# Kernel optimization log

Measured on AMD Instinct MI355X. Metric: run time of the kernel, lower is better.

## Reference

```python
import jax, jax.numpy as jnp
import numpy as np

B, N, C, H = 8, 4096, 512, 8
HD = C // H  # head_dim = 64
SCALE = HD ** -0.5


def setup_inputs() -> dict:
    key = jax.random.key(0)
    k1, k2, k3, k4 = jax.random.split(key, 4)
    x1 = jax.random.normal(k1, (B, N, C), dtype=jnp.float32)
    x2 = jax.random.normal(k2, (B, N, C), dtype=jnp.float32)
    # nn.Linear(dim, 2*dim, bias=False) weights; stored as [in, out] for x @ W
    lim = 1.0 / np.sqrt(C)
    W_kv1 = jax.random.uniform(k3, (C, 2 * C), dtype=jnp.float32, minval=-lim, maxval=lim)
    W_kv2 = jax.random.uniform(k4, (C, 2 * C), dtype=jnp.float32, minval=-lim, maxval=lim)
    return {"x1": x1, "x2": x2, "W_kv1": W_kv1, "W_kv2": W_kv2}


def _heads(t):
    # [B, N, C] -> [B, H, N, HD]
    return t.reshape(B, N, H, HD).transpose(0, 2, 1, 3)


def _kv(x, W):
    kv = (x @ W).reshape(B, N, 2, H, HD)  # [B, N, 2, H, HD]
    kv = kv.transpose(2, 0, 3, 1, 4)      # [2, B, H, N, HD]
    return kv[0], kv[1]


def _ctx(k, v):
    # K^T V: [B, H, HD, HD], scaled then softmax over axis -2 (the k-feature axis)
    ctx = jnp.einsum("bhnd,bhne->bhde", k, v) * SCALE
    return jax.nn.softmax(ctx, axis=-2)


def reference(x1, x2, W_kv1, W_kv2):
    q1 = _heads(x1)
    q2 = _heads(x2)
    k1, v1 = _kv(x1, W_kv1)
    k2, v2 = _kv(x2, W_kv2)
    ctx1 = _ctx(k1, v1)
    ctx2 = _ctx(k2, v2)
    # cross: q1 attends via ctx2, q2 via ctx1
    o1 = jnp.einsum("bhnd,bhde->bhne", q1, ctx2).transpose(0, 2, 1, 3).reshape(B, N, C)
    o2 = jnp.einsum("bhnd,bhde->bhne", q2, ctx1).transpose(0, 2, 1, 3).reshape(B, N, C)
    return o1, o2
```

## Files before the change

### kernel.cpp

```cpp
#include <hip/hip_runtime.h>
#include <stdint.h>
#include <stddef.h>

#define NB 8
#define NSEQ 4096
#define NC 512
#define NH 8

typedef __attribute__((ext_vector_type(4))) float f4;
typedef __attribute__((ext_vector_type(8))) short bf8;
typedef __attribute__((ext_vector_type(4))) short bf4;

__device__ __forceinline__ short f2bf(float f) {
  union { float f; unsigned int u; } v; v.f = f;
  unsigned int u = v.u + 0x7FFFu + ((v.u >> 16) & 1u);
  return (short)(u >> 16);
}
__device__ __forceinline__ float bf2f(short h) {
  union { unsigned int u; float f; } v;
  v.u = ((unsigned int)(unsigned short)h) << 16;
  return v.f;
}

__global__ __launch_bounds__(256) void k_wt(const float* __restrict__ W0,
                                            const float* __restrict__ W1,
                                            short* __restrict__ Wth,
                                            short* __restrict__ Wtl) {
  __shared__ float t[64 * 65];
  int bid = blockIdx.x;
  int ot = bid & 15;
  int ct = (bid >> 4) & 7;
  int s = bid >> 7;
  const float* W = s ? W1 : W0;
  const float* src = W + (size_t)(ct * 64) * 1024 + ot * 64;
  int tid = threadIdx.x;
  int rr = tid >> 4, c4 = (tid & 15) * 4;
#pragma unroll
  for (int p = 0; p < 4; ++p) {
    int c = p * 16 + rr;
    f4 v = *(const f4*)&src[(size_t)c * 1024 + c4];
#pragma unroll
    for (int i = 0; i < 4; ++i) t[(c4 + i) * 65 + c] = v[i];
  }
  __syncthreads();
  size_t obase = (size_t)s * 524288 + (size_t)(ot * 64) * 512 + ct * 64;
#pragma unroll
  for (int p = 0; p < 4; ++p) {
    int o = p * 16 + rr;
    bf4 vh, vl;
#pragma unroll
    for (int i = 0; i < 4; ++i) {
      float v = t[o * 65 + c4 + i];
      short h = f2bf(v);
      vh[i] = h; vl[i] = f2bf(v - bf2f(h));
    }
    *(bf4*)&Wth[obase + (size_t)o * 512 + c4] = vh;
    *(bf4*)&Wtl[obase + (size_t)o * 512 + c4] = vl;
  }
}

__global__ __launch_bounds__(256) void k_xbt(const float* __restrict__ x0,
                                             const float* __restrict__ x1,
                                             short* __restrict__ XbT) {
  __shared__ short t[64 * 64];
  int bx = blockIdx.x;
  int ct = bx & 7;
  int nt = (bx >> 3) & 63;
  int b  = (bx >> 9) & 7;
  int s  = bx >> 12;
  const float* x = s ? x1 : x0;
  const float* xb = x + ((size_t)b * NSEQ + (size_t)nt * 64) * NC + ct * 64;
  int tid = threadIdx.x;
  int tn = tid >> 4;
  int tc = (tid & 15) * 4;
#pragma unroll
  for (int r = 0; r < 4; ++r) {
    int n = tn + r * 16;
    f4 v = *(const f4*)&xb[(size_t)n * NC + tc];
#pragma unroll
    for (int i = 0; i < 4; ++i) {
      int c = tc + i;
      int swz = (c & 7) ^ ((c >> 3) & 7);
      int byteoff = c * 128 + ((n * 2) ^ (swz << 4));
      t[byteoff >> 1] = f2bf(v[i]);
    }
  }
  __syncthreads();
  short* Xp = XbT + ((size_t)(s * 8 + b) * NC + (size_t)ct * 64) * NSEQ + (size_t)nt * 64;
  int ng4 = (tid & 15) * 4;
  int crb = tid >> 4;
#pragma unroll
  for (int r = 0; r < 4; ++r) {
    int cr = crb + r * 16;
    int swz = (cr & 7) ^ ((cr >> 3) & 7);
    int byteoff = cr * 128 + ((ng4 * 2) ^ (swz << 4));
    bf4 vv = *(const bf4*)&t[byteoff >> 1];
    *(bf4*)&Xp[(size_t)cr * NSEQ + ng4] = vv;
  }
}

__global__ __launch_bounds__(256) void k_gram(const short* __restrict__ XbT,
                                              float* __restrict__ G32) {
  __shared__ short Ab[2][64 * 64];
  __shared__ short Bb[2][64 * 64];
  int bid = blockIdx.x;
  int xcd = bid & 7;
  int j = bid >> 3;
  int sb = xcd + ((j >= 36) ? 8 : 0);
  int p = (j >= 36) ? (j - 36) : j;
  int ti = 0;
  while (p >= 8 - ti) { p -= 8 - ti; ++ti; }
  int tj = ti + p;
  int diag = (ti == tj);
  const short* Ar = XbT + ((size_t)sb * NC + ti * 64) * NSEQ;
  const short* Br = XbT + ((size_t)sb * NC + tj * 64) * NSEQ;
  int tid = threadIdx.x;
  int lane = tid & 63;
  int w = tid >> 6;
  int lrow = lane >> 3;
  int lgr = lane & 7;
  int wr = w & 1, wc = w >> 1;
  int mrow = lane & 15;
  int kreg = lane >> 4;
  f4 z = {0.f, 0.f, 0.f, 0.f};
  f4 acc[2][2];
#pragma unroll
  for (int i = 0; i < 2; ++i)
#pragma unroll
    for (int jj = 0; jj < 2; ++jj) acc[i][jj] = z;

  auto stage = [&](int buf, int k0) {
#pragma unroll
    for (int q = 0; q < 2; ++q) {
      int row = q * 32 + w * 8 + lrow;
      int gsw = (lgr ^ lrow) << 3;
      __builtin_amdgcn_global_load_lds((const unsigned int*)(Ar + (size_t)row * NSEQ + k0 + gsw),
                                       (unsigned int*)&Ab[buf][(q * 32 + w * 8) * 64], 16, 0, 0);
      if (!diag)
        __builtin_amdgcn_global_load_lds((const unsigned int*)(Br + (size_t)row * NSEQ + k0 + gsw),
                                         (unsigned int*)&Bb[buf][(q * 32 + w * 8) * 64], 16, 0, 0);
    }
  };
  auto comp = [&](int buf) {
    const short* Abuf = Ab[buf];
    const short* Bbuf = diag ? Ab[buf] : Bb[buf];
#pragma unroll
    for (int kk = 0; kk < 2; ++kk) {
      int gr = kk * 4 + kreg;
      bf8 a[2], b[2];
#pragma unroll
      for (int i = 0; i < 2; ++i) {
        int ra = wr * 32 + i * 16 + mrow;
        a[i] = *(const bf8*)&Abuf[ra * 64 + ((gr ^ (ra & 7)) << 3)];
        int rb2 = wc * 32 + i * 16 + mrow;
        b[i] = *(const bf8*)&Bbuf[rb2 * 64 + ((gr ^ (rb2 & 7)) << 3)];
      }
#pragma unroll
      for (int i = 0; i < 2; ++i)
#pragma unroll
        for (int jj = 0; jj < 2; ++jj)
          acc[i][jj] = __builtin_amdgcn_mfma_f32_16x16x32_bf16(a[i], b[jj], acc[i][jj], 0, 0, 0);
    }
  };

  stage(0, 0);
  __syncthreads();
  int cur = 0;
  for (int it = 0; it < 63; ++it) {
    stage(cur ^ 1, (it + 1) * 64);
    comp(cur);
    __syncthreads();
    cur ^= 1;
  }
  comp(cur);

  float* Gp = G32 + (size_t)sb * NC * NC;
  int rb = ti * 64 + wr * 32 + (lane >> 4) * 4;
  int cb = tj * 64 + wc * 32 + (lane & 15);
#pragma unroll
  for (int i = 0; i < 2; ++i)
#pragma unroll
    for (int jj = 0; jj < 2; ++jj)
#pragma unroll
      for (int r = 0; r < 4; ++r)
        Gp[(size_t)(rb + i * 16 + r) * NC + cb + jj * 16] = acc[i][jj][r];
}

__global__ __launch_bounds__(256) void k_sym(const float* __restrict__ G32,
                                             short* __restrict__ Gh,
                                             short* __restrict__ Gl) {
  __shared__ float t[64 * 65];
  int bid = blockIdx.x;
  int tile = bid & 63;
  int sb = bid >> 6;
  int ti = tile >> 3, tj = tile & 7;
  int tr = ti > tj;
  const float* src = G32 + (size_t)sb * 262144
                   + (tr ? ((size_t)(tj * 64) * 512 + ti * 64)
                         : ((size_t)(ti * 64) * 512 + tj * 64));
  int tid = threadIdx.x;
  int rr = tid >> 4;
  int c4 = (tid & 15) * 4;
#pragma unroll
  for (int p = 0; p < 4; ++p) {
    int r = p * 16 + rr;
    f4 v = *(const f4*)&src[(size_t)r * 512 + c4];
    if (tr) {
#pragma unroll
      for (int i = 0; i < 4; ++i) t[(c4 + i) * 65 + r] = v[i];
    } else {
#pragma unroll
      for (int i = 0; i < 4; ++i) t[r * 65 + c4 + i] = v[i];
    }
  }
  __syncthreads();
  size_t obase = (size_t)sb * 262144 + (size_t)(ti * 64) * 512 + tj * 64;
#pragma unroll
  for (int p = 0; p < 4; ++p) {
    int r = p * 16 + rr;
    bf4 vh, vl;
#pragma unroll
    for (int i = 0; i < 4; ++i) {
      float v = t[r * 65 + c4 + i] * 0.125f;
      short h = f2bf(v);
      vh[i] = h; vl[i] = f2bf(v - bf2f(h));
    }
    *(bf4*)&Gh[obase + (size_t)r * 512 + c4] = vh;
    *(bf4*)&Gl[obase + (size_t)r * 512 + c4] = vl;
  }
}

__global__ __launch_bounds__(256) void k_t(const short* __restrict__ Wth,
                                           const short* __restrict__ Wtl,
                                           const short* __restrict__ Gh,
                                           const short* __restrict__ Gl,
                                           float* __restrict__ Ttf) {
  __shared__ short Ah[128 * 40];
  __shared__ short Al[128 * 40];
  __shared__ short Bh[128 * 40];
  __shared__ short Bl[128 * 40];
  int tid = threadIdx.x;
  int et = blockIdx.x & 3;
  int ct = blockIdx.x >> 2;
  int sb = blockIdx.y;
  int s = sb >> 3;
  const short* Avh = Wth + ((size_t)s * 1024 + 512 + (size_t)et * 128) * NC;
  const short* Avl = Wtl + ((size_t)s * 1024 + 512 + (size_t)et * 128) * NC;
  const short* Gph = Gh + (size_t)sb * 262144 + (size_t)(ct * 128) * 512;
  const short* Gpl = Gl + (size_t)sb * 262144 + (size_t)(ct * 128) * 512;
  int cc = tid >> 1;
  int kh = (tid & 1) * 16;
  int lane = tid & 63;
  int w = tid >> 6;
  int wm = (w & 1) * 64;
  int wn = (w >> 1) * 64;
  int mrow = lane & 15;
  int kcol = (lane >> 4) * 8;
  f4 z = {0.f, 0.f, 0.f, 0.f};
  f4 acc[4][4];
#pragma unroll
  for (int i = 0; i < 4; ++i)
#pragma unroll
    for (int j = 0; j < 4; ++j) acc[i][j] = z;

  for (int it = 0; it < 16; ++it) {
    int k0 = it * 32;
    __syncthreads();
    *(bf8*)&Ah[cc * 40 + kh]     = *(const bf8*)&Avh[(size_t)cc * NC + k0 + kh];
    *(bf8*)&Ah[cc * 40 + kh + 8] = *(const bf8*)&Avh[(size_t)cc * NC + k0 + kh + 8];
    *(bf8*)&Al[cc * 40 + kh]     = *(const bf8*)&Avl[(size_t)cc * NC + k0 + kh];
    *(bf8*)&Al[cc * 40 + kh + 8] = *(const bf8*)&Avl[(size_t)cc * NC + k0 + kh + 8];
    *(bf8*)&Bh[cc * 40 + kh]     = *(const bf8*)&Gph[(size_t)cc * 512 + k0 + kh];
    *(bf8*)&Bh[cc * 40 + kh + 8] = *(const bf8*)&Gph[(size_t)cc * 512 + k0 + kh + 8];
    *(bf8*)&Bl[cc * 40 + kh]     = *(const bf8*)&Gpl[(size_t)cc * 512 + k0 + kh];
    *(bf8*)&Bl[cc * 40 + kh + 8] = *(const bf8*)&Gpl[(size_t)cc * 512 + k0 + kh + 8];
    __syncthreads();
    bf8 ah[4], al[4], bh[4], bl[4];
#pragma unroll
    for (int i = 0; i < 4; ++i) {
      ah[i] = *(const bf8*)&Ah[(wm + i * 16 + mrow) * 40 + kcol];
      al[i] = *(const bf8*)&Al[(wm + i * 16 + mrow) * 40 + kcol];
      bh[i] = *(const bf8*)&Bh[(wn + i * 16 + mrow) * 40 + kcol];
      bl[i] = *(const bf8*)&Bl[(wn + i * 16 + mrow) * 40 + kcol];
    }
#pragma unroll
    for (int i = 0; i < 4; ++i)
#pragma unroll
      for (int j = 0; j < 4; ++j) {
        acc[i][j] = __builtin_amdgcn_mfma_f32_16x16x32_bf16(ah[i], bh[j], acc[i][j], 0, 0, 0);
        acc[i][j] = __builtin_amdgcn_mfma_f32_16x16x32_bf16(ah[i], bl[j], acc[i][j], 0, 0, 0);
        acc[i][j] = __builtin_amdgcn_mfma_f32_16x16x32_bf16(al[i], bh[j], acc[i][j], 0, 0, 0);
      }
  }
  float* Tp = Ttf + (size_t)sb * NC * NC;
  int rb = et * 128 + wm + (lane >> 4) * 4;
  int cb = ct * 128 + wn + (lane & 15);
#pragma unroll
  for (int i = 0; i < 4; ++i)
#pragma unroll
    for (int j = 0; j < 4; ++j)
#pragma unroll
      for (int r = 0; r < 4; ++r)
        Tp[(size_t)(rb + i * 16 + r) * NC + cb + j * 16] = acc[i][j][r];
}

__global__ __launch_bounds__(256) void k_ctx(const short* __restrict__ Wth,
                                             const short* __restrict__ Wtl,
                                             const float* __restrict__ Ttf,
                                             short* __restrict__ ctxT) {
  __shared__ short Ah[64 * 72];
  __shared__ short Al[64 * 72];
  __shared__ short Bh[64 * 72];
  __shared__ short Bl[64 * 72];
  __shared__ float Sf[64 * 68];
  int tid = threadIdx.x;
  int h = blockIdx.x & 7;
  int sb = blockIdx.x >> 3;
  int s = sb >> 3;
  const short* Akh = Wth + ((size_t)s * 1024 + (size_t)h * 64) * NC;
  const short* Akl = Wtl + ((size_t)s * 1024 + (size_t)h * 64) * NC;
  const float* Bt = Ttf + ((size_t)sb * NC + (size_t)h * 64) * NC;
  int cs = tid >> 3;
  int kg = (tid & 7) * 8;
  int lane = tid & 63;
  int w = tid >> 6;
  int mrow = lane & 15;
  int kcol = (lane >> 4) * 8;
  f4 z = {0.f, 0.f, 0.f, 0.f};
  f4 acc[4];
#pragma unroll
  for (int j = 0; j < 4; ++j) acc[j] = z;

  for (int it = 0; it < 8; ++it) {
    int k0 = it * 64;
    __syncthreads();
#pragma unroll
    for (int r = 0; r < 2; ++r) {
      int d = cs + r * 32;
      *(bf8*)&Ah[d * 72 + kg] = *(const bf8*)&Akh[(size_t)d * NC + k0 + kg];
      *(bf8*)&Al[d * 72 + kg] = *(const bf8*)&Akl[(size_t)d * NC + k0 + kg];
      f4 g0 = *(const f4*)&Bt[(size_t)d * NC + k0 + kg];
      f4 g1 = *(const f4*)&Bt[(size_t)d * NC + k0 + kg + 4];
      bf8 vh, vl;
#pragma unroll
      for (int i = 0; i < 4; ++i) {
        short hh = f2bf(g0[i]);
        vh[i] = hh; vl[i] = f2bf(g0[i] - bf2f(hh));
        hh = f2bf(g1[i]);
        vh[i + 4] = hh; vl[i + 4] = f2bf(g1[i] - bf2f(hh));
      }
      *(bf8*)&Bh[d * 72 + kg] = vh;
      *(bf8*)&Bl[d * 72 + kg] = vl;
    }
    __syncthreads();
#pragma unroll
    for (int kk = 0; kk < 2; ++kk) {
      bf8 ah = *(const bf8*)&Ah[(w * 16 + mrow) * 72 + kk * 32 + kcol];
      bf8 al = *(const bf8*)&Al[(w * 16 + mrow) * 72 + kk * 32 + kcol];
#pragma unroll
      for (int j = 0; j < 4; ++j) {
        bf8 bh = *(const bf8*)&Bh[(j * 16 + mrow) * 72 + kk * 32 + kcol];
        bf8 bl = *(const bf8*)&Bl[(j * 16 + mrow) * 72 + kk * 32 + kcol];
        acc[j] = __builtin_amdgcn_mfma_f32_16x16x32_bf16(ah, bh, acc[j], 0, 0, 0);
        acc[j] = __builtin_amdgcn_mfma_f32_16x16x32_bf16(ah, bl, acc[j], 0, 0, 0);
        acc[j] = __builtin_amdgcn_mfma_f32_16x16x32_bf16(al, bh, acc[j], 0, 0, 0);
      }
    }
  }
  __syncthreads();
#pragma unroll
  for (int j = 0; j < 4; ++j)
#pragma unroll
    for (int r = 0; r < 4; ++r)
      Sf[(w * 16 + (lane >> 4) * 4 + r) * 68 + j * 16 + (lane & 15)] = acc[j][r];
  __syncthreads();
  if (tid < 64) {
    int e = tid;
    float mx = -1e30f;
    for (int d = 0; d < 64; ++d) mx = fmaxf(mx, Sf[d * 68 + e]);
    float sum = 0.f;
    for (int d = 0; d < 64; ++d) {
      float ev = __expf(Sf[d * 68 + e] - mx);
      sum += ev;
      Sf[d * 68 + e] = ev;
    }
    float rs = 1.f / sum;
    short* cp = ctxT + (((size_t)sb * NH + h) * 64 + e) * 64;
    for (int d0 = 0; d0 < 64; d0 += 4) {
      bf4 ov;
      ov[0] = f2bf(Sf[(d0 + 0) * 68 + e] * rs);
      ov[1] = f2bf(Sf[(d0 + 1) * 68 + e] * rs);
      ov[2] = f2bf(Sf[(d0 + 2) * 68 + e] * rs);
      ov[3] = f2bf(Sf[(d0 + 3) * 68 + e] * rs);
      *(bf4*)&cp[d0] = ov;
    }
  }
}

__global__ __launch_bounds__(256) void k_o(const float* __restrict__ x0,
                                           const float* __restrict__ x1,
                                           const short* __restrict__ ctxT,
                                           float* __restrict__ out) {
  __shared__ short Ab[128 * 72];
  __shared__ short Bb[64 * 72];
  int tid = threadIdx.x;
  int bx = blockIdx.x;
  int nt = bx & 31;
  int h = (bx >> 5) & 7;
  int b = (bx >> 8) & 7;
  int so = bx >> 11;
  const float* x = so ? x1 : x0;
  const short* cp = ctxT + (((size_t)(1 - so) * NB + b) * NH + h) * 64 * 64;
  {
    int e = tid >> 2;
    int dg = (tid & 3) * 16;
    *(bf8*)&Bb[e * 72 + dg] = *(const bf8*)&cp[e * 64 + dg];
    *(bf8*)&Bb[e * 72 + dg + 8] = *(const bf8*)&cp[e * 64 + dg + 8];
  }
  const float* xp = x + ((size_t)b * NSEQ + (size_t)nt * 128) * NC + h * 64;
  {
    int n = tid >> 1;
    int dh = (tid & 1) * 32;
    const float* row = xp + (size_t)n * NC + dh;
#pragma unroll
    for (int q = 0; q < 4; ++q) {
      f4 v0 = *(const f4*)&row[q * 8];
      f4 v1 = *(const f4*)&row[q * 8 + 4];
      bf8 pv;
      pv[0] = f2bf(v0[0]); pv[1] = f2bf(v0[1]); pv[2] = f2bf(v0[2]); pv[3] = f2bf(v0[3]);
      pv[4] = f2bf(v1[0]); pv[5] = f2bf(v1[1]); pv[6] = f2bf(v1[2]); pv[7] = f2bf(v1[3]);
      *(bf8*)&Ab[n * 72 + dh + q * 8] = pv;
    }
  }
  __syncthreads();
  int lane = tid & 63;
  int w = tid >> 6;
  int mrow = lane & 15;
  int kcol = (lane >> 4) * 8;
  f4 z = {0.f, 0.f, 0.f, 0.f};
  f4 acc[2][4];
#pragma unroll
  for (int i = 0; i < 2; ++i)
#pragma unroll
    for (int j = 0; j < 4; ++j) acc[i][j] = z;
#pragma unroll
  for (int kk = 0; kk < 2; ++kk) {
    bf8 a0 = *(const bf8*)&Ab[(w * 32 + mrow) * 72 + kk * 32 + kcol];
    bf8 a1 = *(const bf8*)&Ab[(w * 32 + 16 + mrow) * 72 + kk * 32 + kcol];
#pragma unroll
    for (int j = 0; j < 4; ++j) {
      bf8 bv = *(const bf8*)&Bb[(j * 16 + mrow) * 72 + kk * 32 + kcol];
      acc[0][j] = __builtin_amdgcn_mfma_f32_16x16x32_bf16(a0, bv, acc[0][j], 0, 0, 0);
      acc[1][j] = __builtin_amdgcn_mfma_f32_16x16x32_bf16(a1, bv, acc[1][j], 0, 0, 0);
    }
  }
  float* op = out + (size_t)so * ((size_t)NB * NSEQ * NC)
            + ((size_t)b * NSEQ + (size_t)nt * 128) * NC + h * 64;
#pragma unroll
  for (int i = 0; i < 2; ++i)
#pragma unroll
    for (int j = 0; j < 4; ++j)
#pragma unroll
      for (int r = 0; r < 4; ++r)
        op[(size_t)(w * 32 + i * 16 + (lane >> 4) * 4 + r) * NC + j * 16 + (lane & 15)] = acc[i][j][r];
}

extern "C" void kernel_launch(void* const* d_in, const int* in_sizes, int n_in,
                              void* d_out, int out_size, void* d_ws, size_t ws_size,
                              hipStream_t stream) {
  const float* x1 = (const float*)d_in[0];
  const float* x2 = (const float*)d_in[1];
  const float* W1 = (const float*)d_in[2];
  const float* W2 = (const float*)d_in[3];
  float* out = (float*)d_out;
  char* ws = (char*)d_ws;
  short* XbT  = (short*)ws;
  float* Ttf  = (float*)ws;
  short* Gh   = (short*)(ws + 16777216);
  short* Gl   = (short*)(ws + 25165824);
  short* Wth  = (short*)(ws + 67108864);
  short* Wtl  = (short*)(ws + 69206016);
  float* G32  = (float*)(ws + 71303168);
  short* ctxT = (short*)(ws + 88080384);

  hipLaunchKernelGGL(k_wt,   dim3(256),   dim3(256), 0, stream, W1, W2, Wth, Wtl);
  hipLaunchKernelGGL(k_xbt,  dim3(8192),  dim3(256), 0, stream, x1, x2, XbT);
  hipLaunchKernelGGL(k_gram, dim3(576),   dim3(256), 0, stream, XbT, G32);
  hipLaunchKernelGGL(k_sym,  dim3(1024),  dim3(256), 0, stream, G32, Gh, Gl);
  hipLaunchKernelGGL(k_t,    dim3(16, 16), dim3(256), 0, stream, Wth, Wtl, Gh, Gl, Ttf);
  hipLaunchKernelGGL(k_ctx,  dim3(128),   dim3(256), 0, stream, Wth, Wtl, Ttf, ctxT);
  hipLaunchKernelGGL(k_o,    dim3(4096),  dim3(256), 0, stream, x1, x2, ctxT, out);
}
```

Measured before the change: 185.5 us.

## Fuse bf16 transpose of x into Gram kernel and use packed bf16 convert

Removes the separate k_xbt kernel that wrote a transposed bf16 copy of x. The Gram kernel now reads fp32 x directly, converts it to bf16 in registers, and stores it transposed and swizzled into LDS, with register-prefetch double buffering replacing the async global-to-LDS loads. This drops a full write and re-read of a 64MB intermediate and one launch. The cost is twice as many global bytes read per Gram tile (fp32 instead of bf16) with redundant reads across tiles, plus extra VGPR pressure. Conversions in the Gram and output kernels now use v_cvt_pk_bf16_f32.

```diff
diff --git a/kernel.cpp b/kernel.cpp
--- a/kernel.cpp
+++ b/kernel.cpp
@@ -10,6 +10,8 @@
 typedef __attribute__((ext_vector_type(4))) float f4;
 typedef __attribute__((ext_vector_type(8))) short bf8;
 typedef __attribute__((ext_vector_type(4))) short bf4;
+typedef __attribute__((ext_vector_type(2))) unsigned int u32x2;
+typedef __attribute__((ext_vector_type(4))) unsigned int u32x4;
 
 __device__ __forceinline__ short f2bf(float f) {
   union { float f; unsigned int u; } v; v.f = f;
@@ -20,6 +22,11 @@
   union { unsigned int u; float f; } v;
   v.u = ((unsigned int)(unsigned short)h) << 16;
   return v.f;
+}
+__device__ __forceinline__ unsigned int cvtpk(float a, float b) {
+  unsigned int r;
+  asm("v_cvt_pk_bf16_f32 %0, %1, %2" : "=v"(r) : "v"(a), "v"(b));
+  return r;
 }
 
 __global__ __launch_bounds__(256) void k_wt(const float* __restrict__ W0,
@@ -59,47 +66,8 @@
   }
 }
 
-__global__ __launch_bounds__(256) void k_xbt(const float* __restrict__ x0,
-                                             const float* __restrict__ x1,
-                                             short* __restrict__ XbT) {
-  __shared__ short t[64 * 64];
-  int bx = blockIdx.x;
-  int ct = bx & 7;
-  int nt = (bx >> 3) & 63;
-  int b  = (bx >> 9) & 7;
-  int s  = bx >> 12;
-  const float* x = s ? x1 : x0;
-  const float* xb = x + ((size_t)b * NSEQ + (size_t)nt * 64) * NC + ct * 64;
-  int tid = threadIdx.x;
-  int tn = tid >> 4;
-  int tc = (tid & 15) * 4;
-#pragma unroll
-  for (int r = 0; r < 4; ++r) {
-    int n = tn + r * 16;
-    f4 v = *(const f4*)&xb[(size_t)n * NC + tc];
-#pragma unroll
-    for (int i = 0; i < 4; ++i) {
-      int c = tc + i;
-      int swz = (c & 7) ^ ((c >> 3) & 7);
-      int byteoff = c * 128 + ((n * 2) ^ (swz << 4));
-      t[byteoff >> 1] = f2bf(v[i]);
-    }
-  }
-  __syncthreads();
-  short* Xp = XbT + ((size_t)(s * 8 + b) * NC + (size_t)ct * 64) * NSEQ + (size_t)nt * 64;
-  int ng4 = (tid & 15) * 4;
-  int crb = tid >> 4;
-#pragma unroll
-  for (int r = 0; r < 4; ++r) {
-    int cr = crb + r * 16;
-    int swz = (cr & 7) ^ ((cr >> 3) & 7);
-    int byteoff = cr * 128 + ((ng4 * 2) ^ (swz << 4));
-    bf4 vv = *(const bf4*)&t[byteoff >> 1];
-    *(bf4*)&Xp[(size_t)cr * NSEQ + ng4] = vv;
-  }
-}
-
-__global__ __launch_bounds__(256) void k_gram(const short* __restrict__ XbT,
+__global__ __launch_bounds__(256) void k_gram(const float* __restrict__ x0,
+                                              const float* __restrict__ x1,
                                               float* __restrict__ G32) {
   __shared__ short Ab[2][64 * 64];
   __shared__ short Bb[2][64 * 64];
@@ -112,13 +80,15 @@
   while (p >= 8 - ti) { p -= 8 - ti; ++ti; }
   int tj = ti + p;
   int diag = (ti == tj);
-  const short* Ar = XbT + ((size_t)sb * NC + ti * 64) * NSEQ;
-  const short* Br = XbT + ((size_t)sb * NC + tj * 64) * NSEQ;
+  int s = sb >> 3, b = sb & 7;
+  const float* x = s ? x1 : x0;
+  const float* Axp = x + (size_t)b * NSEQ * NC + ti * 64;
+  const float* Bxp = x + (size_t)b * NSEQ * NC + tj * 64;
   int tid = threadIdx.x;
   int lane = tid & 63;
   int w = tid >> 6;
-  int lrow = lane >> 3;
-  int lgr = lane & 7;
+  int c4 = (tid & 15) * 4;
+  int n4 = (tid >> 4) * 4;
   int wr = w & 1, wc = w >> 1;
   int mrow = lane & 15;
   int kreg = lane >> 4;
@@ -129,16 +99,32 @@
 #pragma unroll
     for (int jj = 0; jj < 2; ++jj) acc[i][jj] = z;
 
-  auto stage = [&](int buf, int k0) {
-#pragma unroll
-    for (int q = 0; q < 2; ++q) {
-      int row = q * 32 + w * 8 + lrow;
-      int gsw = (lgr ^ lrow) << 3;
-      __builtin_amdgcn_global_load_lds((const unsigned int*)(Ar + (size_t)row * NSEQ + k0 + gsw),
-                                       (unsigned int*)&Ab[buf][(q * 32 + w * 8) * 64], 16, 0, 0);
-      if (!diag)
-        __builtin_amdgcn_global_load_lds((const unsigned int*)(Br + (size_t)row * NSEQ + k0 + gsw),
-                                         (unsigned int*)&Bb[buf][(q * 32 + w * 8) * 64], 16, 0, 0);
+  f4 va[4], vb[4];
+  auto load = [&](int n0) {
+#pragma unroll
+    for (int i = 0; i < 4; ++i)
+      va[i] = *(const f4*)&Axp[(size_t)(n0 + n4 + i) * NC + c4];
+    if (!diag) {
+#pragma unroll
+      for (int i = 0; i < 4; ++i)
+        vb[i] = *(const f4*)&Bxp[(size_t)(n0 + n4 + i) * NC + c4];
+    }
+  };
+  auto store = [&](int buf) {
+#pragma unroll
+    for (int ci = 0; ci < 4; ++ci) {
+      int c = c4 + ci;
+      int soff = c * 64 + ((((n4 >> 3) ^ (c & 7))) << 3) + (n4 & 7);
+      u32x2 wa;
+      wa[0] = cvtpk(va[0][ci], va[1][ci]);
+      wa[1] = cvtpk(va[2][ci], va[3][ci]);
+      *(u32x2*)&Ab[buf][soff] = wa;
+      if (!diag) {
+        u32x2 wb;
+        wb[0] = cvtpk(vb[0][ci], vb[1][ci]);
+        wb[1] = cvtpk(vb[2][ci], vb[3][ci]);
+        *(u32x2*)&Bb[buf][soff] = wb;
+      }
     }
   };
   auto comp = [&](int buf) {
@@ -147,32 +133,35 @@
 #pragma unroll
     for (int kk = 0; kk < 2; ++kk) {
       int gr = kk * 4 + kreg;
-      bf8 a[2], b[2];
+      bf8 a[2], bb[2];
 #pragma unroll
       for (int i = 0; i < 2; ++i) {
         int ra = wr * 32 + i * 16 + mrow;
         a[i] = *(const bf8*)&Abuf[ra * 64 + ((gr ^ (ra & 7)) << 3)];
         int rb2 = wc * 32 + i * 16 + mrow;
-        b[i] = *(const bf8*)&Bbuf[rb2 * 64 + ((gr ^ (rb2 & 7)) << 3)];
+        bb[i] = *(const bf8*)&Bbuf[rb2 * 64 + ((gr ^ (rb2 & 7)) << 3)];
       }
 #pragma unroll
       for (int i = 0; i < 2; ++i)
 #pragma unroll
         for (int jj = 0; jj < 2; ++jj)
-          acc[i][jj] = __builtin_amdgcn_mfma_f32_16x16x32_bf16(a[i], b[jj], acc[i][jj], 0, 0, 0);
+          acc[i][jj] = __builtin_amdgcn_mfma_f32_16x16x32_bf16(a[i], bb[jj], acc[i][jj], 0, 0, 0);
     }
   };
 
-  stage(0, 0);
+  load(0);
+  store(0);
   __syncthreads();
   int cur = 0;
-  for (int it = 0; it < 63; ++it) {
-    stage(cur ^ 1, (it + 1) * 64);
+  for (int it = 0; it < 64; ++it) {
+    if (it < 63) load((it + 1) * 64);
     comp(cur);
-    __syncthreads();
+    if (it < 63) {
+      store(cur ^ 1);
+      __syncthreads();
+    }
     cur ^= 1;
   }
-  comp(cur);
 
   float* Gp = G32 + (size_t)sb * NC * NC;
   int rb = ti * 64 + wr * 32 + (lane >> 4) * 4;
@@ -426,10 +415,12 @@
     for (int q = 0; q < 4; ++q) {
       f4 v0 = *(const f4*)&row[q * 8];
       f4 v1 = *(const f4*)&row[q * 8 + 4];
-      bf8 pv;
-      pv[0] = f2bf(v0[0]); pv[1] = f2bf(v0[1]); pv[2] = f2bf(v0[2]); pv[3] = f2bf(v0[3]);
-      pv[4] = f2bf(v1[0]); pv[5] = f2bf(v1[1]); pv[6] = f2bf(v1[2]); pv[7] = f2bf(v1[3]);
-      *(bf8*)&Ab[n * 72 + dh + q * 8] = pv;
+      u32x4 pw;
+      pw[0] = cvtpk(v0[0], v0[1]);
+      pw[1] = cvtpk(v0[2], v0[3]);
+      pw[2] = cvtpk(v1[0], v1[1]);
+      pw[3] = cvtpk(v1[2], v1[3]);
+      *(u32x4*)&Ab[n * 72 + dh + q * 8] = pw;
     }
   }
   __syncthreads();
@@ -474,7 +465,6 @@
   const float* W2 = (const float*)d_in[3];
   float* out = (float*)d_out;
   char* ws = (char*)d_ws;
-  short* XbT  = (short*)ws;
   float* Ttf  = (float*)ws;
   short* Gh   = (short*)(ws + 16777216);
   short* Gl   = (short*)(ws + 25165824);
@@ -483,11 +473,10 @@
   float* G32  = (float*)(ws + 71303168);
   short* ctxT = (short*)(ws + 88080384);
 
-  hipLaunchKernelGGL(k_wt,   dim3(256),   dim3(256), 0, stream, W1, W2, Wth, Wtl);
-  hipLaunchKernelGGL(k_xbt,  dim3(8192),  dim3(256), 0, stream, x1, x2, XbT);
-  hipLaunchKernelGGL(k_gram, dim3(576),   dim3(256), 0, stream, XbT, G32);
-  hipLaunchKernelGGL(k_sym,  dim3(1024),  dim3(256), 0, stream, G32, Gh, Gl);
+  hipLaunchKernelGGL(k_wt,   dim3(256),    dim3(256), 0, stream, W1, W2, Wth, Wtl);
+  hipLaunchKernelGGL(k_gram, dim3(576),    dim3(256), 0, stream, x1, x2, G32);
+  hipLaunchKernelGGL(k_sym,  dim3(1024),   dim3(256), 0, stream, G32, Gh, Gl);
   hipLaunchKernelGGL(k_t,    dim3(16, 16), dim3(256), 0, stream, Wth, Wtl, Gh, Gl, Ttf);
-  hipLaunchKernelGGL(k_ctx,  dim3(128),   dim3(256), 0, stream, Wth, Wtl, Ttf, ctxT);
-  hipLaunchKernelGGL(k_o,    dim3(4096),  dim3(256), 0, stream, x1, x2, ctxT, out);
-}
+  hipLaunchKernelGGL(k_ctx,  dim3(128),    dim3(256), 0, stream, Wth, Wtl, Ttf, ctxT);
+  hipLaunchKernelGGL(k_o,    dim3(4096),   dim3(256), 0, stream, x1, x2, ctxT, out);
+}
```

After: 222.0 us. 19.6% more time.
